# Optimization experiments

Measured on AMD Instinct MI355X. Metric: run time of the kernel, lower is better.

The kernel has to match this reference:

```python
import jax, jax.numpy as jnp
import numpy as np

T = 2_000_000  # seq_len
I, H, O = 2, 30, 1  # input_size, hidden_size, output_size


def setup_inputs() -> dict:
    key = jax.random.key(0)
    ks = jax.random.split(key, 7)
    s = 1.0 / np.sqrt(H)  # torch default uniform(-1/sqrt(H), 1/sqrt(H)) scale
    return {
        "x": jax.random.normal(ks[0], (T, I), dtype=jnp.float32),
        "W_ih": jax.random.uniform(ks[1], (H, I), jnp.float32, -s, s),
        "W_hh": jax.random.uniform(ks[2], (H, H), jnp.float32, -s, s),
        "b_ih": jax.random.uniform(ks[3], (H,), jnp.float32, -s, s),
        "b_hh": jax.random.uniform(ks[4], (H,), jnp.float32, -s, s),
        "W_fc": jax.random.uniform(ks[5], (O, H), jnp.float32, -s, s),
        "b_fc": jax.random.uniform(ks[6], (O,), jnp.float32, -s, s),
    }


def reference(x, W_ih, W_hh, b_ih, b_hh, W_fc, b_fc):
    # Elman RNN (torch.nn.RNN, tanh): h_t = tanh(x_t W_ih^T + b_ih + h_{t-1} W_hh^T + b_hh)
    # Precompute the input projection for all timesteps in one GEMM.
    xp = x @ W_ih.T + (b_ih + b_hh)  # [T, H]

    def step(h, xt):
        h = jnp.tanh(xt + h @ W_hh.T)
        return h, h

    h0 = jnp.zeros((H,), dtype=x.dtype)
    _, hs = jax.lax.scan(step, h0, xp)  # hs: [T, H]
    return hs @ W_fc.T + b_fc  # [T, O]
```

## Files before the change

kernel.cpp:

```cpp
#include <hip/hip_runtime.h>


#define T_LEN     2000000
#define HID       30
#define CHUNK_LEN 32
#define BURN      23
#define NBLOCK    512
#define WSTEPS    8
#define NWIN      7

typedef __attribute__((ext_vector_type(4))) _Float16 half4;
typedef __attribute__((ext_vector_type(2))) __fp16   fp16x2;
typedef __attribute__((ext_vector_type(4))) float    float4v;

union h4u { half4 v4; fp16x2 v2[2]; unsigned u2[2]; };
union h2u { fp16x2 v; unsigned u; };

#define STAGE_LOAD(o) {                                                      \
    const int tb = st_base_t + (o) * WSTEPS;                                 \
    int i0 = tb + st_j,     i1 = tb + st_j + 1;                              \
    int i2 = tb + st_j + 4, i3 = tb + st_j + 5;                              \
    i0 = i0 < 0 ? 0 : (i0 >= T_LEN ? T_LEN - 1 : i0);                        \
    i1 = i1 < 0 ? 0 : (i1 >= T_LEN ? T_LEN - 1 : i1);                        \
    i2 = i2 < 0 ? 0 : (i2 >= T_LEN ? T_LEN - 1 : i2);                        \
    i3 = i3 < 0 ? 0 : (i3 >= T_LEN ? T_LEN - 1 : i3);                        \
    stv0 = ((const float2*)x)[i0]; stv1 = ((const float2*)x)[i1];            \
    stv2 = ((const float2*)x)[i2]; stv3 = ((const float2*)x)[i3];            \
}
#define STAGE_WRITE(o) {                                                     \
    const int wb = ((o) & 1) * 1024;                                         \
    h2u c0, c1, c2, c3;                                                      \
    c0.v = __builtin_amdgcn_cvt_pkrtz(stv0.x, stv0.y);                       \
    c1.v = __builtin_amdgcn_cvt_pkrtz(stv1.x, stv1.y);                       \
    c2.v = __builtin_amdgcn_cvt_pkrtz(stv2.x, stv2.y);                       \
    c3.v = __builtin_amdgcn_cvt_pkrtz(stv3.x, stv3.y);                       \
    lds_x[wb + (st_j + 0) * 128 + st_c] = c0.u;                              \
    lds_x[wb + (st_j + 1) * 128 + st_c] = c1.u;                              \
    lds_x[wb + (st_j + 4) * 128 + st_c] = c2.u;                              \
    lds_x[wb + (st_j + 5) * 128 + st_c] = c3.u;                              \
}

#define STEP_BODY(s, MASKQ, STOREQ)                                          \
{                                                                            \
    const unsigned xcA = lds_x[rbA + (s) * 128];                             \
    const unsigned xcB = lds_x[rbB + (s) * 128];                             \
    float tA[8], tB[8];                                                      \
    _Pragma("unroll")                                                        \
    for (int i = 0; i < 4; ++i) {                                            \
        tA[i]   = 1.f - 2.f * __builtin_amdgcn_rcpf(1.f + __builtin_amdgcn_exp2f(d_tA[i])); \
        tA[4+i] = 1.f - 2.f * __builtin_amdgcn_rcpf(1.f + __builtin_amdgcn_exp2f(d_bA[i])); \
        tB[i]   = 1.f - 2.f * __builtin_amdgcn_rcpf(1.f + __builtin_amdgcn_exp2f(d_tB[i])); \
        tB[4+i] = 1.f - 2.f * __builtin_amdgcn_rcpf(1.f + __builtin_amdgcn_exp2f(d_bB[i])); \
    }                                                                        \
    if (MASKQ) {                                                             \
        \
        const float m = (t_cur >= 1) ? 1.f : 0.f;                            \
        _Pragma("unroll")                                                    \
        for (int i = 0; i < 8; ++i) tA[i] *= m;                              \
    }                                                                        \
    h4u b0A, b1A, b0B, b1B;                                                  \
    b0A.v2[0] = __builtin_amdgcn_cvt_pkrtz(tA[0], tA[1]);                    \
    b0A.v2[1] = __builtin_amdgcn_cvt_pkrtz(tA[2], tA[3]);                    \
    b1A.v2[0] = __builtin_amdgcn_cvt_pkrtz(tA[4], tA[5]);                    \
    b1A.v2[1] = __builtin_amdgcn_cvt_pkrtz(tA[6], tA[7]);                    \
    b0B.v2[0] = __builtin_amdgcn_cvt_pkrtz(tB[0], tB[1]);                    \
    b0B.v2[1] = __builtin_amdgcn_cvt_pkrtz(tB[2], tB[3]);                    \
    b1B.v2[0] = __builtin_amdgcn_cvt_pkrtz(tB[4], tB[5]);                    \
    b1B.v2[1] = __builtin_amdgcn_cvt_pkrtz(tB[6], tB[7]);                    \
    if (g3) { b1A.u2[1] = xcA; b1B.u2[1] = xcB; }                            \
    d_tA = __builtin_amdgcn_mfma_f32_16x16x16f16(a_t0, b0A.v4, cT, 0, 0, 0); \
    d_bA = __builtin_amdgcn_mfma_f32_16x16x16f16(a_b0, b0A.v4, cB, 0, 0, 0); \
    d_tB = __builtin_amdgcn_mfma_f32_16x16x16f16(a_t0, b0B.v4, cT, 0, 0, 0); \
    d_bB = __builtin_amdgcn_mfma_f32_16x16x16f16(a_b0, b0B.v4, cB, 0, 0, 0); \
    d_tA = __builtin_amdgcn_mfma_f32_16x16x16f16(a_t1, b1A.v4, d_tA, 0, 0, 0); \
    d_bA = __builtin_amdgcn_mfma_f32_16x16x16f16(a_b1, b1A.v4, d_bA, 0, 0, 0); \
    d_tB = __builtin_amdgcn_mfma_f32_16x16x16f16(a_t1, b1B.v4, d_tB, 0, 0, 0); \
    d_bB = __builtin_amdgcn_mfma_f32_16x16x16f16(a_b1, b1B.v4, d_bB, 0, 0, 0); \
    if (STOREQ) {                                                            \
        const int ta = t_cur - 1;                                            \
        if (g3 && ta < my_endA) out[ta] = d_bA[2];                           \
        const int tb2 = ta + 16 * CHUNK_LEN;                                 \
        if (g3 && tb2 < my_endB) out[tb2] = d_bB[2];                         \
    }                                                                        \
    ++t_cur;                                                                 \
}

__global__ __launch_bounds__(256, 2)
void rnn_mfma_kernel(const float* __restrict__ x,
                     const float* __restrict__ W_ih,
                     const float* __restrict__ W_hh,
                     const float* __restrict__ b_ih,
                     const float* __restrict__ b_hh,
                     const float* __restrict__ W_fc,
                     const float* __restrict__ b_fc,
                     float* __restrict__ out)
{
    __shared__ unsigned lds_x[2 * WSTEPS * 128];

    const int tid  = threadIdx.x;
    const int wave = tid >> 6;
    const int lane = tid & 63;
    const int g    = lane >> 4;
    const int cl   = lane & 15;
    const bool g3  = (g == 3);

    const int rdA = wave * 32 + cl;
    const int rdB = rdA + 16;
    const int chunkA = blockIdx.x * 128 + rdA;
    const int chunkB = chunkA + 16;

    const int st_c = tid >> 1;
    const int st_j = (tid & 1) * 2;
    const int st_base_t = (blockIdx.x * 128 + st_c) * CHUNK_LEN - BURN;

    const float SC = 2.0f * 1.44269504088896340736f;

    half4 a_t0, a_t1, a_b0, a_b1;
#pragma unroll
    for (int i = 0; i < 4; ++i) {
        const int k0 = 4*g + i;
        const int k1 = 16 + 4*g + i;
        const int mt = cl;
        const int mb = 16 + cl;

        a_t0[i] = (_Float16)(SC * W_hh[mt*HID + k0]);
        float v_t1;
        if (k1 < HID)        v_t1 = SC * W_hh[mt*HID + k1];
        else if (k1 == HID)  v_t1 = SC * W_ih[mt*2 + 0];
        else                 v_t1 = SC * W_ih[mt*2 + 1];
        a_t1[i] = (_Float16)v_t1;

        float v_b0, v_b1;
        if (mb < HID) {
            v_b0 = SC * W_hh[mb*HID + k0];
            if (k1 < HID)        v_b1 = SC * W_hh[mb*HID + k1];
            else if (k1 == HID)  v_b1 = SC * W_ih[mb*2 + 0];
            else                 v_b1 = SC * W_ih[mb*2 + 1];
        } else if (mb == HID) {
            v_b0 = W_fc[k0];
            v_b1 = (k1 < HID) ? W_fc[k1] : 0.f;
        } else {
            v_b0 = 0.f; v_b1 = 0.f;
        }
        a_b0[i] = (_Float16)v_b0;
        a_b1[i] = (_Float16)v_b1;
    }

    float4v cT, cB;
#pragma unroll
    for (int i = 0; i < 4; ++i) {
        const int rt  = 4*g + i;
        const int rb2 = 16 + 4*g + i;
        cT[i] = SC * (b_ih[rt] + b_hh[rt]);
        cB[i] = (rb2 < HID)  ? SC * (b_ih[rb2] + b_hh[rb2])
              : (rb2 == HID) ? b_fc[0] : 0.f;
    }

    int my_endA = chunkA * CHUNK_LEN + CHUNK_LEN;
    if (my_endA > T_LEN) my_endA = T_LEN;
    int my_endB = chunkB * CHUNK_LEN + CHUNK_LEN;
    if (my_endB > T_LEN) my_endB = T_LEN;

    __builtin_amdgcn_sched_barrier(0);

    float4v d_tA = {0.f,0.f,0.f,0.f}, d_bA = {0.f,0.f,0.f,0.f};
    float4v d_tB = {0.f,0.f,0.f,0.f}, d_bB = {0.f,0.f,0.f,0.f};

    int t_cur = chunkA * CHUNK_LEN - BURN;

    float2 stv0, stv1, stv2, stv3;
    STAGE_LOAD(0)
    STAGE_WRITE(0)
    __syncthreads();

#pragma clang loop unroll(disable)
    for (int o = 0; o < 3; ++o) {
        const int wb  = (o & 1) * 1024;
        const int rbA = wb + rdA, rbB = wb + rdB;
        STAGE_LOAD(o + 1)
#pragma clang loop unroll(disable)
        for (int s = 0; s < WSTEPS; ++s) {
            STEP_BODY(s, true, false)
        }
        STAGE_WRITE(o + 1)
        __syncthreads();
    }

#pragma clang loop unroll(disable)
    for (int o = 3; o < NWIN; ++o) {
        const int wb  = (o & 1) * 1024;
        const int rbA = wb + rdA, rbB = wb + rdB;
        if (o < NWIN - 1) STAGE_LOAD(o + 1)
#pragma clang loop unroll(disable)
        for (int s = 0; s < WSTEPS; ++s) {
            STEP_BODY(s, false, true)
        }
        if (o < NWIN - 1) STAGE_WRITE(o + 1)
        __syncthreads();
    }
}

extern "C" void kernel_launch(void* const* d_in, const int* in_sizes, int n_in,
                              void* d_out, int out_size, void* d_ws, size_t ws_size,
                              hipStream_t stream)
{
    const float* x    = (const float*)d_in[0];
    const float* W_ih = (const float*)d_in[1];
    const float* W_hh = (const float*)d_in[2];
    const float* b_ih = (const float*)d_in[3];
    const float* b_hh = (const float*)d_in[4];
    const float* W_fc = (const float*)d_in[5];
    const float* b_fc = (const float*)d_in[6];
    float* out = (float*)d_out;

    rnn_mfma_kernel<<<NBLOCK, 256, 0, stream>>>(x, W_ih, W_hh, b_ih, b_hh,
                                                W_fc, b_fc, out);
}
```

Baseline: 106.3 us.

## Drop dual-chunk interleave per wave and use longer chunks with shorter burn-in

Each wave now runs a single set of 16 recurrence chunks instead of two interleaved sets. Chunks grow from 32 to 64 timesteps, and the warm-up burn-in drops from 23 to 15 steps. The LDS staging buffer and loader indexing are halved to match, and the per-step MFMA and tanh work is halved. In exchange the wave loses the second independent dependency chain that hid MFMA and transcendental latency, and it runs more sequential steps (80 instead of 56). The shorter burn-in may also reduce accuracy at chunk boundaries.

```diff
diff --git a/kernel.cpp b/kernel.cpp
--- a/kernel.cpp
+++ b/kernel.cpp
@@ -3,11 +3,11 @@
 
 #define T_LEN     2000000
 #define HID       30
-#define CHUNK_LEN 32
-#define BURN      23
+#define CHUNK_LEN 64
+#define BURN      15
 #define NBLOCK    512
 #define WSTEPS    8
-#define NWIN      7
+#define NWIN      10
 
 typedef __attribute__((ext_vector_type(4))) _Float16 half4;
 typedef __attribute__((ext_vector_type(2))) __fp16   fp16x2;
@@ -18,69 +18,49 @@
 
 #define STAGE_LOAD(o) {                                                      \
     const int tb = st_base_t + (o) * WSTEPS;                                 \
-    int i0 = tb + st_j,     i1 = tb + st_j + 1;                              \
-    int i2 = tb + st_j + 4, i3 = tb + st_j + 5;                              \
+    int i0 = tb + st_j;                                                      \
+    int i1 = tb + st_j + 4;                                                  \
     i0 = i0 < 0 ? 0 : (i0 >= T_LEN ? T_LEN - 1 : i0);                        \
     i1 = i1 < 0 ? 0 : (i1 >= T_LEN ? T_LEN - 1 : i1);                        \
-    i2 = i2 < 0 ? 0 : (i2 >= T_LEN ? T_LEN - 1 : i2);                        \
-    i3 = i3 < 0 ? 0 : (i3 >= T_LEN ? T_LEN - 1 : i3);                        \
-    stv0 = ((const float2*)x)[i0]; stv1 = ((const float2*)x)[i1];            \
-    stv2 = ((const float2*)x)[i2]; stv3 = ((const float2*)x)[i3];            \
+    stv0 = ((const float2*)x)[i0];                                           \
+    stv1 = ((const float2*)x)[i1];                                           \
 }
 #define STAGE_WRITE(o) {                                                     \
-    const int wb = ((o) & 1) * 1024;                                         \
-    h2u c0, c1, c2, c3;                                                      \
+    const int wb = ((o) & 1) * 512;                                          \
+    h2u c0, c1;                                                              \
     c0.v = __builtin_amdgcn_cvt_pkrtz(stv0.x, stv0.y);                       \
     c1.v = __builtin_amdgcn_cvt_pkrtz(stv1.x, stv1.y);                       \
-    c2.v = __builtin_amdgcn_cvt_pkrtz(stv2.x, stv2.y);                       \
-    c3.v = __builtin_amdgcn_cvt_pkrtz(stv3.x, stv3.y);                       \
-    lds_x[wb + (st_j + 0) * 128 + st_c] = c0.u;                              \
-    lds_x[wb + (st_j + 1) * 128 + st_c] = c1.u;                              \
-    lds_x[wb + (st_j + 4) * 128 + st_c] = c2.u;                              \
-    lds_x[wb + (st_j + 5) * 128 + st_c] = c3.u;                              \
+    lds_x[wb + (st_j + 0) * 64 + st_c] = c0.u;                               \
+    lds_x[wb + (st_j + 4) * 64 + st_c] = c1.u;                               \
 }
 
 #define STEP_BODY(s, MASKQ, STOREQ)                                          \
 {                                                                            \
-    const unsigned xcA = lds_x[rbA + (s) * 128];                             \
-    const unsigned xcB = lds_x[rbB + (s) * 128];                             \
-    float tA[8], tB[8];                                                      \
+    const unsigned xc = lds_x[rbA + (s) * 64];                               \
+    float th[8];                                                             \
     _Pragma("unroll")                                                        \
     for (int i = 0; i < 4; ++i) {                                            \
-        tA[i]   = 1.f - 2.f * __builtin_amdgcn_rcpf(1.f + __builtin_amdgcn_exp2f(d_tA[i])); \
-        tA[4+i] = 1.f - 2.f * __builtin_amdgcn_rcpf(1.f + __builtin_amdgcn_exp2f(d_bA[i])); \
-        tB[i]   = 1.f - 2.f * __builtin_amdgcn_rcpf(1.f + __builtin_amdgcn_exp2f(d_tB[i])); \
-        tB[4+i] = 1.f - 2.f * __builtin_amdgcn_rcpf(1.f + __builtin_amdgcn_exp2f(d_bB[i])); \
+        th[i]   = 1.f - 2.f * __builtin_amdgcn_rcpf(1.f + __builtin_amdgcn_exp2f(d_t[i])); \
+        th[4+i] = 1.f - 2.f * __builtin_amdgcn_rcpf(1.f + __builtin_amdgcn_exp2f(d_b[i])); \
     }                                                                        \
     if (MASKQ) {                                                             \
-        \
         const float m = (t_cur >= 1) ? 1.f : 0.f;                            \
         _Pragma("unroll")                                                    \
-        for (int i = 0; i < 8; ++i) tA[i] *= m;                              \
+        for (int i = 0; i < 8; ++i) th[i] *= m;                              \
     }                                                                        \
-    h4u b0A, b1A, b0B, b1B;                                                  \
-    b0A.v2[0] = __builtin_amdgcn_cvt_pkrtz(tA[0], tA[1]);                    \
-    b0A.v2[1] = __builtin_amdgcn_cvt_pkrtz(tA[2], tA[3]);                    \
-    b1A.v2[0] = __builtin_amdgcn_cvt_pkrtz(tA[4], tA[5]);                    \
-    b1A.v2[1] = __builtin_amdgcn_cvt_pkrtz(tA[6], tA[7]);                    \
-    b0B.v2[0] = __builtin_amdgcn_cvt_pkrtz(tB[0], tB[1]);                    \
-    b0B.v2[1] = __builtin_amdgcn_cvt_pkrtz(tB[2], tB[3]);                    \
-    b1B.v2[0] = __builtin_amdgcn_cvt_pkrtz(tB[4], tB[5]);                    \
-    b1B.v2[1] = __builtin_amdgcn_cvt_pkrtz(tB[6], tB[7]);                    \
-    if (g3) { b1A.u2[1] = xcA; b1B.u2[1] = xcB; }                            \
-    d_tA = __builtin_amdgcn_mfma_f32_16x16x16f16(a_t0, b0A.v4, cT, 0, 0, 0); \
-    d_bA = __builtin_amdgcn_mfma_f32_16x16x16f16(a_b0, b0A.v4, cB, 0, 0, 0); \
-    d_tB = __builtin_amdgcn_mfma_f32_16x16x16f16(a_t0, b0B.v4, cT, 0, 0, 0); \
-    d_bB = __builtin_amdgcn_mfma_f32_16x16x16f16(a_b0, b0B.v4, cB, 0, 0, 0); \
-    d_tA = __builtin_amdgcn_mfma_f32_16x16x16f16(a_t1, b1A.v4, d_tA, 0, 0, 0); \
-    d_bA = __builtin_amdgcn_mfma_f32_16x16x16f16(a_b1, b1A.v4, d_bA, 0, 0, 0); \
-    d_tB = __builtin_amdgcn_mfma_f32_16x16x16f16(a_t1, b1B.v4, d_tB, 0, 0, 0); \
-    d_bB = __builtin_amdgcn_mfma_f32_16x16x16f16(a_b1, b1B.v4, d_bB, 0, 0, 0); \
+    h4u b0, b1;                                                              \
+    b0.v2[0] = __builtin_amdgcn_cvt_pkrtz(th[0], th[1]);                     \
+    b0.v2[1] = __builtin_amdgcn_cvt_pkrtz(th[2], th[3]);                     \
+    b1.v2[0] = __builtin_amdgcn_cvt_pkrtz(th[4], th[5]);                     \
+    b1.v2[1] = __builtin_amdgcn_cvt_pkrtz(th[6], th[7]);                     \
+    if (g3) b1.u2[1] = xc;                                                   \
+    d_t = __builtin_amdgcn_mfma_f32_16x16x16f16(a_t0, b0.v4, cT, 0, 0, 0);   \
+    d_b = __builtin_amdgcn_mfma_f32_16x16x16f16(a_b0, b0.v4, cB, 0, 0, 0);   \
+    d_t = __builtin_amdgcn_mfma_f32_16x16x16f16(a_t1, b1.v4, d_t, 0, 0, 0);  \
+    d_b = __builtin_amdgcn_mfma_f32_16x16x16f16(a_b1, b1.v4, d_b, 0, 0, 0);  \
     if (STOREQ) {                                                            \
         const int ta = t_cur - 1;                                            \
-        if (g3 && ta < my_endA) out[ta] = d_bA[2];                           \
-        const int tb2 = ta + 16 * CHUNK_LEN;                                 \
-        if (g3 && tb2 < my_endB) out[tb2] = d_bB[2];                         \
+        if (g3 && ta < my_end) out[ta] = d_b[2];                             \
     }                                                                        \
     ++t_cur;                                                                 \
 }
@@ -95,7 +75,7 @@
                      const float* __restrict__ b_fc,
                      float* __restrict__ out)
 {
-    __shared__ unsigned lds_x[2 * WSTEPS * 128];
+    __shared__ unsigned lds_x[2 * WSTEPS * 64];
 
     const int tid  = threadIdx.x;
     const int wave = tid >> 6;
@@ -104,14 +84,12 @@
     const int cl   = lane & 15;
     const bool g3  = (g == 3);
 
-    const int rdA = wave * 32 + cl;
-    const int rdB = rdA + 16;
-    const int chunkA = blockIdx.x * 128 + rdA;
-    const int chunkB = chunkA + 16;
+    const int rdA   = wave * 16 + cl;
+    const int chunk = blockIdx.x * 64 + rdA;
 
-    const int st_c = tid >> 1;
-    const int st_j = (tid & 1) * 2;
-    const int st_base_t = (blockIdx.x * 128 + st_c) * CHUNK_LEN - BURN;
+    const int st_c = tid >> 2;
+    const int st_j = tid & 3;
+    const int st_base_t = (blockIdx.x * 64 + st_c) * CHUNK_LEN - BURN;
 
     const float SC = 2.0f * 1.44269504088896340736f;
 
@@ -156,27 +134,23 @@
               : (rb2 == HID) ? b_fc[0] : 0.f;
     }
 
-    int my_endA = chunkA * CHUNK_LEN + CHUNK_LEN;
-    if (my_endA > T_LEN) my_endA = T_LEN;
-    int my_endB = chunkB * CHUNK_LEN + CHUNK_LEN;
-    if (my_endB > T_LEN) my_endB = T_LEN;
+    int my_end = chunk * CHUNK_LEN + CHUNK_LEN;
+    if (my_end > T_LEN) my_end = T_LEN;
 
     __builtin_amdgcn_sched_barrier(0);
 
-    float4v d_tA = {0.f,0.f,0.f,0.f}, d_bA = {0.f,0.f,0.f,0.f};
-    float4v d_tB = {0.f,0.f,0.f,0.f}, d_bB = {0.f,0.f,0.f,0.f};
+    float4v d_t = {0.f,0.f,0.f,0.f}, d_b = {0.f,0.f,0.f,0.f};
 
-    int t_cur = chunkA * CHUNK_LEN - BURN;
+    int t_cur = chunk * CHUNK_LEN - BURN;
 
-    float2 stv0, stv1, stv2, stv3;
+    float2 stv0, stv1;
     STAGE_LOAD(0)
     STAGE_WRITE(0)
     __syncthreads();
 
 #pragma clang loop unroll(disable)
-    for (int o = 0; o < 3; ++o) {
-        const int wb  = (o & 1) * 1024;
-        const int rbA = wb + rdA, rbB = wb + rdB;
+    for (int o = 0; o < 2; ++o) {
+        const int rbA = (o & 1) * 512 + rdA;
         STAGE_LOAD(o + 1)
 #pragma clang loop unroll(disable)
         for (int s = 0; s < WSTEPS; ++s) {
@@ -187,9 +161,8 @@
     }
 
 #pragma clang loop unroll(disable)
-    for (int o = 3; o < NWIN; ++o) {
-        const int wb  = (o & 1) * 1024;
-        const int rbA = wb + rdA, rbB = wb + rdB;
+    for (int o = 2; o < NWIN; ++o) {
+        const int rbA = (o & 1) * 512 + rdA;
         if (o < NWIN - 1) STAGE_LOAD(o + 1)
 #pragma clang loop unroll(disable)
         for (int s = 0; s < WSTEPS; ++s) {
```

Measured after the change: 99.60 us. -6.3%, faster.
